# Kernel optimization log

Hardware: AMD Instinct MI355X
Metric: run time of the kernel (lower is better)

## Reference

```python
import jax, jax.numpy as jnp
import numpy as np

N, E, D_IN, D_H, D_OUT = 50000, 640000, 128, 128, 64
EPS = 1e-5


def _sage(x, src, dst, Wl, bl, Wr):
    # PyG SAGEConv: out = lin_l(mean_{j in N(i)} x_j) + lin_r(x_i)
    msg = x[src]                                             # [E, d] gather
    agg = jax.ops.segment_sum(msg, dst, num_segments=x.shape[0])
    deg = jax.ops.segment_sum(jnp.ones((src.shape[0],), x.dtype), dst,
                              num_segments=x.shape[0])
    agg = agg / jnp.maximum(deg, 1.0)[:, None]               # mean aggregate
    return agg @ Wl + bl + x @ Wr


def _bn_eval(x, gamma, beta, mean, var):
    return (x - mean) * jax.lax.rsqrt(var + EPS) * gamma + beta


def setup_inputs() -> dict:
    key = jax.random.key(0)
    ks = jax.random.split(key, 16)
    s = lambda d: 1.0 / np.sqrt(d)
    inp = {
        "x": jax.random.normal(ks[0], (N, D_IN), jnp.float32),
        "edge_index": jax.random.randint(ks[1], (2, E), 0, N, jnp.int64),
        # layer 0: 128 -> 128
        "Wl0": jax.random.normal(ks[2], (D_IN, D_H), jnp.float32) * s(D_IN),
        "bl0": jnp.zeros((D_H,), jnp.float32),
        "Wr0": jax.random.normal(ks[3], (D_IN, D_H), jnp.float32) * s(D_IN),
        # layer 1: 128 -> 128
        "Wl1": jax.random.normal(ks[4], (D_H, D_H), jnp.float32) * s(D_H),
        "bl1": jnp.zeros((D_H,), jnp.float32),
        "Wr1": jax.random.normal(ks[5], (D_H, D_H), jnp.float32) * s(D_H),
        # layer 2: 128 -> 64
        "Wl2": jax.random.normal(ks[6], (D_H, D_OUT), jnp.float32) * s(D_H),
        "bl2": jnp.zeros((D_OUT,), jnp.float32),
        "Wr2": jax.random.normal(ks[7], (D_H, D_OUT), jnp.float32) * s(D_H),
        # BatchNorm (eval mode) for the two hidden layers
        "g0": jnp.ones((D_H,), jnp.float32),
        "b0": jnp.zeros((D_H,), jnp.float32),
        "m0": jax.random.normal(ks[8], (D_H,), jnp.float32) * 0.1,
        "v0": jax.random.uniform(ks[9], (D_H,), jnp.float32, 0.5, 1.5),
        "g1": jnp.ones((D_H,), jnp.float32),
        "b1": jnp.zeros((D_H,), jnp.float32),
        "m1": jax.random.normal(ks[10], (D_H,), jnp.float32) * 0.1,
        "v1": jax.random.uniform(ks[11], (D_H,), jnp.float32, 0.5, 1.5),
    }
    return inp


def reference(x, edge_index, Wl0, bl0, Wr0, Wl1, bl1, Wr1, Wl2, bl2, Wr2,
              g0, b0, m0, v0, g1, b1, m1, v1):
    src, dst = edge_index[0], edge_index[1]
    # edge mask (edge_index < N) is all-true by construction -> no-op
    h = _sage(x, src, dst, Wl0, bl0, Wr0)
    h = jax.nn.relu(_bn_eval(h, g0, b0, m0, v0))   # eval: dropout is identity
    h = _sage(h, src, dst, Wl1, bl1, Wr1)
    h = jax.nn.relu(_bn_eval(h, g1, b1, m1, v1))
    h = _sage(h, src, dst, Wl2, bl2, Wr2)
    return jax.nn.log_softmax(h, axis=1)
```

## Files before the change

### kernel.cpp

```cpp
#include <hip/hip_runtime.h>

#define EPS 1e-5f
#define ELL_CAP 64

typedef __attribute__((ext_vector_type(8))) short short8;
typedef __attribute__((ext_vector_type(4))) float f32x4;

__device__ inline unsigned short f2b(float f) {
    union { float f; unsigned u; } v; v.f = f;
    unsigned u = v.u;
    return (unsigned short)((u + 0x7fffu + ((u >> 16) & 1u)) >> 16);
}
__device__ inline float b2f(unsigned short u) {
    union { unsigned u; float f; } v;
    v.u = ((unsigned)u) << 16;
    return v.f;
}


__device__ inline void cvt_one(const float* Wl, const float* Wr,
                               unsigned short* BT, int dout, int idx) {
    int n = idx >> 7, k = idx & 127;
    float w = (n < dout) ? Wl[k * dout + n] : Wr[k * dout + (n - dout)];
    BT[idx] = f2b(w);
}

__global__ void k_cvt_w3(const float* __restrict__ Wl0, const float* __restrict__ Wr0,
                         const float* __restrict__ Wl1, const float* __restrict__ Wr1,
                         const float* __restrict__ Wl2, const float* __restrict__ Wr2,
                         unsigned short* __restrict__ BT0,
                         unsigned short* __restrict__ BT1,
                         unsigned short* __restrict__ BT2) {
    int idx = blockIdx.x * blockDim.x + threadIdx.x;
    const int S0 = 256 * 128, S1 = 256 * 128, S2 = 128 * 128;
    if (idx < S0) cvt_one(Wl0, Wr0, BT0, 128, idx);
    else if (idx < S0 + S1) cvt_one(Wl1, Wr1, BT1, 128, idx - S0);
    else if (idx < S0 + S1 + S2) cvt_one(Wl2, Wr2, BT2, 64, idx - S0 - S1);
}


__global__ void k_build_ell(const int* __restrict__ src, const int* __restrict__ dst,
                            int E, int* __restrict__ cnt, int* __restrict__ ell) {
    int i = blockIdx.x * blockDim.x + threadIdx.x;
    int T = gridDim.x * blockDim.x;
    int e0 = i, e1 = i + T, e2 = i + 2 * T, e3 = i + 3 * T;
    int d0 = 0, d1 = 0, d2 = 0, d3 = 0;
    int s0 = 0, s1 = 0, s2 = 0, s3 = 0;
    if (e0 < E) { d0 = dst[e0]; s0 = src[e0]; }
    if (e1 < E) { d1 = dst[e1]; s1 = src[e1]; }
    if (e2 < E) { d2 = dst[e2]; s2 = src[e2]; }
    if (e3 < E) { d3 = dst[e3]; s3 = src[e3]; }
    int p0 = 0, p1 = 0, p2 = 0, p3 = 0;
    if (e0 < E) p0 = atomicAdd(&cnt[d0], 1);
    if (e1 < E) p1 = atomicAdd(&cnt[d1], 1);
    if (e2 < E) p2 = atomicAdd(&cnt[d2], 1);
    if (e3 < E) p3 = atomicAdd(&cnt[d3], 1);
    if (e0 < E && p0 < ELL_CAP) ell[(size_t)d0 * ELL_CAP + p0] = s0;
    if (e1 < E && p1 < ELL_CAP) ell[(size_t)d1 * ELL_CAP + p1] = s1;
    if (e2 < E && p2 < ELL_CAP) ell[(size_t)d2 * ELL_CAP + p2] = s2;
    if (e3 < E && p3 < ELL_CAP) ell[(size_t)d3 * ELL_CAP + p3] = s3;
}


__device__ inline short8 pack8(float4 a, float4 b) {
    short8 r;
    r[0] = (short)f2b(a.x); r[1] = (short)f2b(a.y);
    r[2] = (short)f2b(a.z); r[3] = (short)f2b(a.w);
    r[4] = (short)f2b(b.x); r[5] = (short)f2b(b.y);
    r[6] = (short)f2b(b.z); r[7] = (short)f2b(b.w);
    return r;
}

template <int NCOLS, bool A32>
__global__ void k_mgemm_lds(const void* __restrict__ Av,
                            const unsigned short* __restrict__ BT,
                            unsigned short* __restrict__ C,
                            int M) {
    __shared__ __align__(16) unsigned short Bs[8 * 4 * 64 * 8];

    const int tid  = threadIdx.x;
    const int lane = tid & 63;
    const int wave = tid >> 6;
    const int m16  = lane & 15;
    const int q    = lane >> 4;
    const int row0 = (blockIdx.x * 4 + wave) * 16;
    const int col0 = blockIdx.y * 128;

#pragma unroll
    for (int i = 0; i < 8; ++i) {
        int f   = tid + i * 256;
        int t   = f >> 8;
        int kc  = (f >> 6) & 3;
        int ln  = f & 63;
        int bm  = ln & 15, bq = ln >> 4;
        const short8* gp = (const short8*)(BT + (size_t)(col0 + t * 16 + bm) * 128
                                              + kc * 32 + bq * 8);
        *(short8*)(Bs + (size_t)f * 8) = *gp;
    }

    int arow = row0 + m16;
    if (arow >= M) arow = M - 1;
    short8 af0, af1, af2, af3;
    if (A32) {
        const float4* Ap = (const float4*)((const float*)Av + (size_t)arow * 128 + q * 8);
        af0 = pack8(Ap[0],  Ap[1]);
        af1 = pack8(Ap[8],  Ap[9]);
        af2 = pack8(Ap[16], Ap[17]);
        af3 = pack8(Ap[24], Ap[25]);
    } else {
        const short8* Ap = (const short8*)((const unsigned short*)Av + (size_t)arow * 128 + q * 8);
        af0 = Ap[0]; af1 = Ap[4]; af2 = Ap[8]; af3 = Ap[12];
    }

    __syncthreads();

    f32x4 acc[8] = {};
#pragma unroll
    for (int t = 0; t < 8; ++t) {
        const short8* bp = (const short8*)(Bs + (size_t)(t * 4) * 64 * 8 + (size_t)lane * 8);
        short8 b0 = bp[0];
        short8 b1 = bp[64];
        short8 b2 = bp[128];
        short8 b3 = bp[192];
        acc[t] = __builtin_amdgcn_mfma_f32_16x16x32_bf16(af0, b0, acc[t], 0, 0, 0);
        acc[t] = __builtin_amdgcn_mfma_f32_16x16x32_bf16(af1, b1, acc[t], 0, 0, 0);
        acc[t] = __builtin_amdgcn_mfma_f32_16x16x32_bf16(af2, b2, acc[t], 0, 0, 0);
        acc[t] = __builtin_amdgcn_mfma_f32_16x16x32_bf16(af3, b3, acc[t], 0, 0, 0);
    }

#pragma unroll
    for (int r = 0; r < 4; ++r) {
        int row = row0 + q * 4 + r;
        if (row < M) {
            unsigned short* cp = C + (size_t)row * NCOLS + col0 + m16;
#pragma unroll
            for (int t = 0; t < 8; ++t) cp[t * 16] = f2b(acc[t][r]);
        }
    }
}


__global__ void k_agg128(const unsigned short* __restrict__ PQ,
                         const int* __restrict__ cnt,
                         const int* __restrict__ ell,
                         const float* __restrict__ bl,
                         const float* __restrict__ g, const float* __restrict__ b,
                         const float* __restrict__ m, const float* __restrict__ v,
                         unsigned short* __restrict__ out, int n) {
    int node = (blockIdx.x * blockDim.x + threadIdx.x) >> 6;
    int lane = threadIdx.x & 63;
    if (node >= n) return;
    const ushort2* PQ2 = (const ushort2*)PQ;
    int cn  = cnt[node];
    int deg = min(cn, ELL_CAP);
    int myidx = (lane < deg) ? ell[(size_t)node * ELL_CAP + lane] : 0;
    float sx0 = 0.f, sy0 = 0.f, sx1 = 0.f, sy1 = 0.f;
    int j = 0;
    for (; j + 4 <= deg; j += 4) {
        int i0 = __shfl(myidx, j + 0);
        int i1 = __shfl(myidx, j + 1);
        int i2 = __shfl(myidx, j + 2);
        int i3 = __shfl(myidx, j + 3);
        ushort2 p0 = PQ2[(size_t)i0 * 128 + lane];
        ushort2 p1 = PQ2[(size_t)i1 * 128 + lane];
        ushort2 p2 = PQ2[(size_t)i2 * 128 + lane];
        ushort2 p3 = PQ2[(size_t)i3 * 128 + lane];
        sx0 += b2f(p0.x) + b2f(p1.x); sy0 += b2f(p0.y) + b2f(p1.y);
        sx1 += b2f(p2.x) + b2f(p3.x); sy1 += b2f(p2.y) + b2f(p3.y);
    }
    for (; j < deg; ++j) {
        int sn = __shfl(myidx, j);
        ushort2 p = PQ2[(size_t)sn * 128 + lane];
        sx0 += b2f(p.x); sy0 += b2f(p.y);
    }
    float sx = sx0 + sx1, sy = sy0 + sy1;
    float dg = fmaxf((float)cn, 1.f);
    ushort2 qv = PQ2[(size_t)node * 128 + 64 + lane];
    int c0 = lane * 2;
    float z0 = sx / dg + b2f(qv.x) + bl[c0];
    float z1 = sy / dg + b2f(qv.y) + bl[c0 + 1];
    z0 = (z0 - m[c0]) * rsqrtf(v[c0] + EPS) * g[c0] + b[c0];
    z1 = (z1 - m[c0 + 1]) * rsqrtf(v[c0 + 1] + EPS) * g[c0 + 1] + b[c0 + 1];
    ushort2 r;
    r.x = f2b(fmaxf(z0, 0.f));
    r.y = f2b(fmaxf(z1, 0.f));
    ((ushort2*)out)[(size_t)node * 64 + lane] = r;
}


__global__ void k_agg64(const unsigned short* __restrict__ PQ,
                        const int* __restrict__ cnt,
                        const int* __restrict__ ell,
                        const float* __restrict__ bl,
                        float* __restrict__ out, int n) {
    int node = (blockIdx.x * blockDim.x + threadIdx.x) >> 6;
    int lane = threadIdx.x & 63;
    if (node >= n) return;
    int cn  = cnt[node];
    int deg = min(cn, ELL_CAP);
    int myidx = (lane < deg) ? ell[(size_t)node * ELL_CAP + lane] : 0;
    float s0 = 0.f, s1 = 0.f;
    int j = 0;
    for (; j + 4 <= deg; j += 4) {
        int i0 = __shfl(myidx, j + 0);
        int i1 = __shfl(myidx, j + 1);
        int i2 = __shfl(myidx, j + 2);
        int i3 = __shfl(myidx, j + 3);
        float p0 = b2f(PQ[(size_t)i0 * 128 + lane]);
        float p1 = b2f(PQ[(size_t)i1 * 128 + lane]);
        float p2 = b2f(PQ[(size_t)i2 * 128 + lane]);
        float p3 = b2f(PQ[(size_t)i3 * 128 + lane]);
        s0 += p0 + p1;
        s1 += p2 + p3;
    }
    for (; j < deg; ++j) {
        int sn = __shfl(myidx, j);
        s0 += b2f(PQ[(size_t)sn * 128 + lane]);
    }
    float s = s0 + s1;
    float dg = fmaxf((float)cn, 1.f);
    float z = s / dg + b2f(PQ[(size_t)node * 128 + 64 + lane]) + bl[lane];
    float mx = z;
#pragma unroll
    for (int off = 32; off > 0; off >>= 1) mx = fmaxf(mx, __shfl_xor(mx, off));
    float ex = __expf(z - mx);
    float sm = ex;
#pragma unroll
    for (int off = 32; off > 0; off >>= 1) sm += __shfl_xor(sm, off);
    out[(size_t)node * 64 + lane] = z - mx - __logf(sm);
}


extern "C" void kernel_launch(void* const* d_in, const int* in_sizes, int n_in,
                              void* d_out, int out_size, void* d_ws, size_t ws_size,
                              hipStream_t stream) {
    const float* x   = (const float*)d_in[0];
    const int*   ei  = (const int*)d_in[1];
    const float* Wl0 = (const float*)d_in[2];
    const float* bl0 = (const float*)d_in[3];
    const float* Wr0 = (const float*)d_in[4];
    const float* Wl1 = (const float*)d_in[5];
    const float* bl1 = (const float*)d_in[6];
    const float* Wr1 = (const float*)d_in[7];
    const float* Wl2 = (const float*)d_in[8];
    const float* bl2 = (const float*)d_in[9];
    const float* Wr2 = (const float*)d_in[10];
    const float* g0  = (const float*)d_in[11];
    const float* b0  = (const float*)d_in[12];
    const float* m0  = (const float*)d_in[13];
    const float* v0  = (const float*)d_in[14];
    const float* g1  = (const float*)d_in[15];
    const float* b1  = (const float*)d_in[16];
    const float* m1  = (const float*)d_in[17];
    const float* v1  = (const float*)d_in[18];

    const int N = in_sizes[0] / 128;
    const int E = in_sizes[1] / 2;
    const int* src = ei;
    const int* dst = ei + E;

    size_t off = 0;
    auto alloc = [&](size_t bytes) -> void* {
        void* p = (char*)d_ws + off;
        off += (bytes + 255) & ~(size_t)255;
        return p;
    };
    int* cnt = (int*)alloc((size_t)N * 4);
    int* ell = (int*)alloc((size_t)N * ELL_CAP * 4);
    unsigned short* PQ  = (unsigned short*)alloc((size_t)N * 256 * 2);
    unsigned short* hb  = (unsigned short*)alloc((size_t)N * 128 * 2);
    unsigned short* BT0 = (unsigned short*)alloc((size_t)256 * 128 * 2);
    unsigned short* BT1 = (unsigned short*)alloc((size_t)256 * 128 * 2);
    unsigned short* BT2 = (unsigned short*)alloc((size_t)128 * 128 * 2);
    (void)ws_size;

    const int CVT_TOTAL = 256 * 128 + 256 * 128 + 128 * 128;
    k_cvt_w3<<<(CVT_TOTAL + 255) / 256, 256, 0, stream>>>(
        Wl0, Wr0, Wl1, Wr1, Wl2, Wr2, BT0, BT1, BT2);

    hipMemsetAsync(cnt, 0, (size_t)N * 4, stream);
    int buildThreads = (E + 3) / 4;
    k_build_ell<<<(buildThreads + 255) / 256, 256, 0, stream>>>(src, dst, E, cnt, ell);

    int rowBlocks = (N + 63) / 64;
    dim3 mg2(rowBlocks, 2);
    dim3 mg1(rowBlocks, 1);
    int aggGrid = (N + 3) / 4;

    k_mgemm_lds<256, true><<<mg2, 256, 0, stream>>>(x, BT0, PQ, N);
    k_agg128<<<aggGrid, 256, 0, stream>>>(PQ, cnt, ell, bl0, g0, b0, m0, v0, hb, N);
    k_mgemm_lds<256, false><<<mg2, 256, 0, stream>>>(hb, BT1, PQ, N);
    k_agg128<<<aggGrid, 256, 0, stream>>>(PQ, cnt, ell, bl1, g1, b1, m1, v1, hb, N);
    k_mgemm_lds<128, false><<<mg1, 256, 0, stream>>>(hb, BT2, PQ, N);
    k_agg64<<<aggGrid, 256, 0, stream>>>(PQ, cnt, ell, bl2, (float*)d_out, N);
}
```

Before: 270.5 us.

## Use 16-bit ELL indices, vectorized multi-edge gathers, fold cnt memset into weight cast

Neighbor indices in the ELL table are stored as 16-bit values, halving index traffic. This is only valid if node ids fit in 16 bits, and N=50000 does. The aggregation kernels now load ushort4 per lane, so each wave processes 2 (or 4) edges per gather with a cross-half shuffle reduction, and the epilogues are vectorized. The separate memset of the degree counters is folded into the weight-conversion kernel to remove one launch, which relies on that grid covering N threads.

```diff
diff --git a/kernel.cpp b/kernel.cpp
--- a/kernel.cpp
+++ b/kernel.cpp
@@ -30,9 +30,11 @@
                          const float* __restrict__ Wl2, const float* __restrict__ Wr2,
                          unsigned short* __restrict__ BT0,
                          unsigned short* __restrict__ BT1,
-                         unsigned short* __restrict__ BT2) {
+                         unsigned short* __restrict__ BT2,
+                         int* __restrict__ cnt, int N) {
     int idx = blockIdx.x * blockDim.x + threadIdx.x;
     const int S0 = 256 * 128, S1 = 256 * 128, S2 = 128 * 128;
+    if (idx < N) cnt[idx] = 0;
     if (idx < S0) cvt_one(Wl0, Wr0, BT0, 128, idx);
     else if (idx < S0 + S1) cvt_one(Wl1, Wr1, BT1, 128, idx - S0);
     else if (idx < S0 + S1 + S2) cvt_one(Wl2, Wr2, BT2, 64, idx - S0 - S1);
@@ -40,7 +42,8 @@
 
 
 __global__ void k_build_ell(const int* __restrict__ src, const int* __restrict__ dst,
-                            int E, int* __restrict__ cnt, int* __restrict__ ell) {
+                            int E, int* __restrict__ cnt,
+                            unsigned short* __restrict__ ell) {
     int i = blockIdx.x * blockDim.x + threadIdx.x;
     int T = gridDim.x * blockDim.x;
     int e0 = i, e1 = i + T, e2 = i + 2 * T, e3 = i + 3 * T;
@@ -55,10 +58,10 @@
     if (e1 < E) p1 = atomicAdd(&cnt[d1], 1);
     if (e2 < E) p2 = atomicAdd(&cnt[d2], 1);
     if (e3 < E) p3 = atomicAdd(&cnt[d3], 1);
-    if (e0 < E && p0 < ELL_CAP) ell[(size_t)d0 * ELL_CAP + p0] = s0;
-    if (e1 < E && p1 < ELL_CAP) ell[(size_t)d1 * ELL_CAP + p1] = s1;
-    if (e2 < E && p2 < ELL_CAP) ell[(size_t)d2 * ELL_CAP + p2] = s2;
-    if (e3 < E && p3 < ELL_CAP) ell[(size_t)d3 * ELL_CAP + p3] = s3;
+    if (e0 < E && p0 < ELL_CAP) ell[(size_t)d0 * ELL_CAP + p0] = (unsigned short)s0;
+    if (e1 < E && p1 < ELL_CAP) ell[(size_t)d1 * ELL_CAP + p1] = (unsigned short)s1;
+    if (e2 < E && p2 < ELL_CAP) ell[(size_t)d2 * ELL_CAP + p2] = (unsigned short)s2;
+    if (e3 < E && p3 < ELL_CAP) ell[(size_t)d3 * ELL_CAP + p3] = (unsigned short)s3;
 }
 
 
@@ -142,7 +145,7 @@
 
 __global__ void k_agg128(const unsigned short* __restrict__ PQ,
                          const int* __restrict__ cnt,
-                         const int* __restrict__ ell,
+                         const unsigned short* __restrict__ ell,
                          const float* __restrict__ bl,
                          const float* __restrict__ g, const float* __restrict__ b,
                          const float* __restrict__ m, const float* __restrict__ v,
@@ -150,47 +153,62 @@
     int node = (blockIdx.x * blockDim.x + threadIdx.x) >> 6;
     int lane = threadIdx.x & 63;
     if (node >= n) return;
-    const ushort2* PQ2 = (const ushort2*)PQ;
     int cn  = cnt[node];
     int deg = min(cn, ELL_CAP);
-    int myidx = (lane < deg) ? ell[(size_t)node * ELL_CAP + lane] : 0;
-    float sx0 = 0.f, sy0 = 0.f, sx1 = 0.f, sy1 = 0.f;
+    int myidx = (lane < deg) ? (int)ell[(size_t)node * ELL_CAP + lane] : 0;
+    const int half = lane >> 5, hl = lane & 31;
+
+    float a0 = 0.f, a1 = 0.f, a2 = 0.f, a3 = 0.f;
     int j = 0;
     for (; j + 4 <= deg; j += 4) {
-        int i0 = __shfl(myidx, j + 0);
-        int i1 = __shfl(myidx, j + 1);
-        int i2 = __shfl(myidx, j + 2);
-        int i3 = __shfl(myidx, j + 3);
-        ushort2 p0 = PQ2[(size_t)i0 * 128 + lane];
-        ushort2 p1 = PQ2[(size_t)i1 * 128 + lane];
-        ushort2 p2 = PQ2[(size_t)i2 * 128 + lane];
-        ushort2 p3 = PQ2[(size_t)i3 * 128 + lane];
-        sx0 += b2f(p0.x) + b2f(p1.x); sy0 += b2f(p0.y) + b2f(p1.y);
-        sx1 += b2f(p2.x) + b2f(p3.x); sy1 += b2f(p2.y) + b2f(p3.y);
-    }
-    for (; j < deg; ++j) {
-        int sn = __shfl(myidx, j);
-        ushort2 p = PQ2[(size_t)sn * 128 + lane];
-        sx0 += b2f(p.x); sy0 += b2f(p.y);
-    }
-    float sx = sx0 + sx1, sy = sy0 + sy1;
+        int ia = __shfl(myidx, j + half);
+        int ib = __shfl(myidx, j + 2 + half);
+        ushort4 pa = *(const ushort4*)(PQ + (size_t)ia * 256 + 4 * hl);
+        ushort4 pb = *(const ushort4*)(PQ + (size_t)ib * 256 + 4 * hl);
+        a0 += b2f(pa.x) + b2f(pb.x);
+        a1 += b2f(pa.y) + b2f(pb.y);
+        a2 += b2f(pa.z) + b2f(pb.z);
+        a3 += b2f(pa.w) + b2f(pb.w);
+    }
+    for (; j < deg; j += 2) {
+        int rem = deg - j;
+        int ia = __shfl(myidx, min(j + half, deg - 1));
+        if (half == 0 || rem >= 2) {
+            ushort4 pa = *(const ushort4*)(PQ + (size_t)ia * 256 + 4 * hl);
+            a0 += b2f(pa.x); a1 += b2f(pa.y); a2 += b2f(pa.z); a3 += b2f(pa.w);
+        }
+    }
+    a0 += __shfl_xor(a0, 32);
+    a1 += __shfl_xor(a1, 32);
+    a2 += __shfl_xor(a2, 32);
+    a3 += __shfl_xor(a3, 32);
+
     float dg = fmaxf((float)cn, 1.f);
-    ushort2 qv = PQ2[(size_t)node * 128 + 64 + lane];
-    int c0 = lane * 2;
-    float z0 = sx / dg + b2f(qv.x) + bl[c0];
-    float z1 = sy / dg + b2f(qv.y) + bl[c0 + 1];
-    z0 = (z0 - m[c0]) * rsqrtf(v[c0] + EPS) * g[c0] + b[c0];
-    z1 = (z1 - m[c0 + 1]) * rsqrtf(v[c0 + 1] + EPS) * g[c0 + 1] + b[c0 + 1];
-    ushort2 r;
-    r.x = f2b(fmaxf(z0, 0.f));
-    r.y = f2b(fmaxf(z1, 0.f));
-    ((ushort2*)out)[(size_t)node * 64 + lane] = r;
+    ushort4 qv = *(const ushort4*)(PQ + (size_t)node * 256 + 128 + 4 * hl);
+    int c0 = 4 * hl;
+    float4 blv = *(const float4*)(bl + c0);
+    float4 mv  = *(const float4*)(m + c0);
+    float4 vv  = *(const float4*)(v + c0);
+    float4 gv  = *(const float4*)(g + c0);
+    float4 bv  = *(const float4*)(b + c0);
+    float z0 = (a0 / dg + b2f(qv.x) + blv.x - mv.x) * rsqrtf(vv.x + EPS) * gv.x + bv.x;
+    float z1 = (a1 / dg + b2f(qv.y) + blv.y - mv.y) * rsqrtf(vv.y + EPS) * gv.y + bv.y;
+    float z2 = (a2 / dg + b2f(qv.z) + blv.z - mv.z) * rsqrtf(vv.z + EPS) * gv.z + bv.z;
+    float z3 = (a3 / dg + b2f(qv.w) + blv.w - mv.w) * rsqrtf(vv.w + EPS) * gv.w + bv.w;
+    if (half == 0) {
+        ushort4 r;
+        r.x = f2b(fmaxf(z0, 0.f));
+        r.y = f2b(fmaxf(z1, 0.f));
+        r.z = f2b(fmaxf(z2, 0.f));
+        r.w = f2b(fmaxf(z3, 0.f));
+        *(ushort4*)(out + (size_t)node * 128 + c0) = r;
+    }
 }
 
 
 __global__ void k_agg64(const unsigned short* __restrict__ PQ,
                         const int* __restrict__ cnt,
-                        const int* __restrict__ ell,
+                        const unsigned short* __restrict__ ell,
                         const float* __restrict__ bl,
                         float* __restrict__ out, int n) {
     int node = (blockIdx.x * blockDim.x + threadIdx.x) >> 6;
@@ -198,36 +216,54 @@
     if (node >= n) return;
     int cn  = cnt[node];
     int deg = min(cn, ELL_CAP);
-    int myidx = (lane < deg) ? ell[(size_t)node * ELL_CAP + lane] : 0;
-    float s0 = 0.f, s1 = 0.f;
+    int myidx = (lane < deg) ? (int)ell[(size_t)node * ELL_CAP + lane] : 0;
+    const int qtr = lane >> 4, ql = lane & 15;
+
+    float a0 = 0.f, a1 = 0.f, a2 = 0.f, a3 = 0.f;
     int j = 0;
-    for (; j + 4 <= deg; j += 4) {
-        int i0 = __shfl(myidx, j + 0);
-        int i1 = __shfl(myidx, j + 1);
-        int i2 = __shfl(myidx, j + 2);
-        int i3 = __shfl(myidx, j + 3);
-        float p0 = b2f(PQ[(size_t)i0 * 128 + lane]);
-        float p1 = b2f(PQ[(size_t)i1 * 128 + lane]);
-        float p2 = b2f(PQ[(size_t)i2 * 128 + lane]);
-        float p3 = b2f(PQ[(size_t)i3 * 128 + lane]);
-        s0 += p0 + p1;
-        s1 += p2 + p3;
-    }
-    for (; j < deg; ++j) {
-        int sn = __shfl(myidx, j);
-        s0 += b2f(PQ[(size_t)sn * 128 + lane]);
-    }
-    float s = s0 + s1;
+    for (; j + 8 <= deg; j += 8) {
+        int ia = __shfl(myidx, j + qtr);
+        int ib = __shfl(myidx, j + 4 + qtr);
+        ushort4 pa = *(const ushort4*)(PQ + (size_t)ia * 128 + 4 * ql);
+        ushort4 pb = *(const ushort4*)(PQ + (size_t)ib * 128 + 4 * ql);
+        a0 += b2f(pa.x) + b2f(pb.x);
+        a1 += b2f(pa.y) + b2f(pb.y);
+        a2 += b2f(pa.z) + b2f(pb.z);
+        a3 += b2f(pa.w) + b2f(pb.w);
+    }
+    for (; j < deg; j += 4) {
+        int rem = deg - j;
+        int ia = __shfl(myidx, min(j + qtr, deg - 1));
+        if (qtr < rem) {
+            ushort4 pa = *(const ushort4*)(PQ + (size_t)ia * 128 + 4 * ql);
+            a0 += b2f(pa.x); a1 += b2f(pa.y); a2 += b2f(pa.z); a3 += b2f(pa.w);
+        }
+    }
+    a0 += __shfl_xor(a0, 16); a0 += __shfl_xor(a0, 32);
+    a1 += __shfl_xor(a1, 16); a1 += __shfl_xor(a1, 32);
+    a2 += __shfl_xor(a2, 16); a2 += __shfl_xor(a2, 32);
+    a3 += __shfl_xor(a3, 16); a3 += __shfl_xor(a3, 32);
+
     float dg = fmaxf((float)cn, 1.f);
-    float z = s / dg + b2f(PQ[(size_t)node * 128 + 64 + lane]) + bl[lane];
-    float mx = z;
-#pragma unroll
-    for (int off = 32; off > 0; off >>= 1) mx = fmaxf(mx, __shfl_xor(mx, off));
-    float ex = __expf(z - mx);
-    float sm = ex;
-#pragma unroll
-    for (int off = 32; off > 0; off >>= 1) sm += __shfl_xor(sm, off);
-    out[(size_t)node * 64 + lane] = z - mx - __logf(sm);
+    ushort4 qv = *(const ushort4*)(PQ + (size_t)node * 128 + 64 + 4 * ql);
+    int c0 = 4 * ql;
+    float4 blv = *(const float4*)(bl + c0);
+    float z0 = a0 / dg + b2f(qv.x) + blv.x;
+    float z1 = a1 / dg + b2f(qv.y) + blv.y;
+    float z2 = a2 / dg + b2f(qv.z) + blv.z;
+    float z3 = a3 / dg + b2f(qv.w) + blv.w;
+
+    float mx = fmaxf(fmaxf(z0, z1), fmaxf(z2, z3));
+#pragma unroll
+    for (int off = 8; off > 0; off >>= 1) mx = fmaxf(mx, __shfl_xor(mx, off));
+    float sm = __expf(z0 - mx) + __expf(z1 - mx) + __expf(z2 - mx) + __expf(z3 - mx);
+#pragma unroll
+    for (int off = 8; off > 0; off >>= 1) sm += __shfl_xor(sm, off);
+    float lg = mx + __logf(sm);
+    if (qtr == 0) {
+        float4 o = make_float4(z0 - lg, z1 - lg, z2 - lg, z3 - lg);
+        *(float4*)(out + (size_t)node * 64 + c0) = o;
+    }
 }
 
 
@@ -266,7 +302,7 @@
         return p;
     };
     int* cnt = (int*)alloc((size_t)N * 4);
-    int* ell = (int*)alloc((size_t)N * ELL_CAP * 4);
+    unsigned short* ell = (unsigned short*)alloc((size_t)N * ELL_CAP * 2);
     unsigned short* PQ  = (unsigned short*)alloc((size_t)N * 256 * 2);
     unsigned short* hb  = (unsigned short*)alloc((size_t)N * 128 * 2);
     unsigned short* BT0 = (unsigned short*)alloc((size_t)256 * 128 * 2);
@@ -276,9 +312,8 @@
 
     const int CVT_TOTAL = 256 * 128 + 256 * 128 + 128 * 128;
     k_cvt_w3<<<(CVT_TOTAL + 255) / 256, 256, 0, stream>>>(
-        Wl0, Wr0, Wl1, Wr1, Wl2, Wr2, BT0, BT1, BT2);
-
-    hipMemsetAsync(cnt, 0, (size_t)N * 4, stream);
+        Wl0, Wr0, Wl1, Wr1, Wl2, Wr2, BT0, BT1, BT2, cnt, N);
+
     int buildThreads = (E + 3) / 4;
     k_build_ell<<<(buildThreads + 255) / 256, 256, 0, stream>>>(src, dst, E, cnt, ell);
 
```

Result: no change. 268.2 us (-0.9%).
